# Performance work log

Hardware: AMD Instinct MI355X
Metric: run time of the kernel (lower is better)

The kernel has to match this reference:

```python
import jax, jax.numpy as jnp
import numpy as np

NEG_INF = -1e9


def setup_inputs() -> dict:
    key = jax.random.key(0)
    ks = jax.random.split(key, 12)
    B, Tq, Tki, E, D, M = 4, 2048, 2048, 1024, 128, 16384
    return {
        "x": jax.random.normal(ks[0], (B, Tq, E), jnp.float32),
        "ki": jax.random.normal(ks[1], (B, Tki, E), jnp.float32),
        "vi": jax.random.normal(ks[2], (B, Tki, E), jnp.float32),
        "mem_keys": jax.random.normal(ks[3], (B, M, D), jnp.float32),
        "mem_vals": jax.random.normal(ks[4], (B, M, D), jnp.float32),
        "Wq": jax.random.normal(ks[5], (E, D), jnp.float32) / np.sqrt(E),
        "bq": jax.random.normal(ks[6], (D,), jnp.float32) * 0.02,
        "Wk": jax.random.normal(ks[7], (E, D), jnp.float32) / np.sqrt(E),
        "bk": jax.random.normal(ks[8], (D,), jnp.float32) * 0.02,
        "Wv": jax.random.normal(ks[9], (E, D), jnp.float32) / np.sqrt(E),
        "bv": jax.random.normal(ks[10], (D,), jnp.float32) * 0.02,
        "gate": jax.random.normal(ks[11], (1,), jnp.float32),
        "idx": 3,
    }


def reference(x, ki, vi, mem_keys, mem_vals, Wq, bq, Wk, bk, Wv, bv, gate, idx):
    B, Tq, E = x.shape
    D = Wq.shape[1]
    top_k = 32
    q = x @ Wq + bq            # [B,Tq,D]
    k = x @ Wk + bk            # [B,Tq,D]
    v = x @ Wv + bv
    s = idx * D                # idx is a python int -> static slice
    k_full = jnp.concatenate([ki[:, :, s:s + D], k], axis=1)   # [B,Tk,D]
    v_full = jnp.concatenate([vi[:, :, s:s + D], v], axis=1)
    Tk = k_full.shape[1]
    # causal SDPA over prefix+current, offset diagonal Tk-Tq
    scores = jnp.einsum("bqd,bkd->bqk", q, k_full) / jnp.sqrt(jnp.float32(D))
    i = jnp.arange(Tq)[:, None]
    j = jnp.arange(Tk)[None, :]
    causal = j <= i + (Tk - Tq)
    scores = jnp.where(causal, scores, NEG_INF)
    att = jax.nn.softmax(scores, axis=-1)
    out = jnp.einsum("bqk,bkd->bqd", att, v_full)              # [B,Tq,D]
    # kNN memory attention: exact top-k inner-product search per query
    mem_scores = jnp.einsum("btd,bmd->btm", q, mem_keys)       # [B,Tq,M]
    _, top_idx = jax.lax.top_k(mem_scores, top_k)              # [B,Tq,K]
    gather = jax.vmap(lambda mem, ix: mem[ix])                 # per batch
    mem_k = gather(mem_keys, top_idx)                          # [B,Tq,K,D]
    mem_v = gather(mem_vals, top_idx)
    # note: original scales by sqrt(Cq)=sqrt(n_embd), not sqrt(head_size)
    mem_att = jax.nn.softmax(
        jnp.einsum("btd,btkd->btk", q, mem_k) / jnp.sqrt(jnp.float32(E)), axis=-1)
    mem_out = jnp.einsum("btk,btkd->btd", mem_att, mem_v)      # [B,Tq,D]
    md_out = out * gate + mem_out * (1.0 - gate)
    return md_out
```

## Files before the change

### kernel.cpp

```cpp
#include <hip/hip_runtime.h>


using bf16x8 = __attribute__((ext_vector_type(8))) short;
using f32x4  = __attribute__((ext_vector_type(4))) float;

typedef __attribute__((address_space(1))) const void GVoid;
typedef __attribute__((address_space(3))) void LVoid;
__device__ __forceinline__ void gl16(const ushort* g, ushort* l) {
  __builtin_amdgcn_global_load_lds((GVoid*)g, (LVoid*)l, 16, 0, 0);
}

__device__ __forceinline__ float bf2f(ushort h) {
  union { uint u; float f; } x; x.u = ((uint)h) << 16; return x.f;
}
__device__ __forceinline__ ushort f2bf(float f) {
  union { float f; uint u; } x; x.f = f;
  uint u = x.u;
  u += 0x7fffu + ((u >> 16) & 1u);
  return (ushort)(u >> 16);
}
__device__ __forceinline__ uint ord2(uint v) {
  uint lo = v & 0xffffu, hi = v >> 16;
  lo = (lo & 0x8000u) ? (0xffffu ^ lo) : (lo | 0x8000u);
  hi = (hi & 0x8000u) ? (0xffffu ^ hi) : (hi | 0x8000u);
  return lo | (hi << 16);
}

__global__ __launch_bounds__(256) void k_wt(const float* __restrict__ Wq,
                                            const float* __restrict__ Wk,
                                            const float* __restrict__ Wv,
                                            ushort* __restrict__ Wth,
                                            ushort* __restrict__ Wtlq) {
  int id = blockIdx.x * 256 + threadIdx.x;
  int z = id >> 17, r = id & 131071;
  int n = r >> 10, k = r & 1023;
  const float* W = (z == 1) ? Wk : (z == 2) ? Wv : Wq;
  float w = W[k * 128 + n];
  ushort h = f2bf(w);
  if (z < 3) Wth[id] = h;
  else       Wtlq[r] = f2bf(w - bf2f(h));
}

__global__ __launch_bounds__(256) void k_cvt8(const float* __restrict__ src,
                                              ushort* __restrict__ dst) {
  int id = blockIdx.x * 256 + threadIdx.x;
  size_t base = (size_t)id * 8;
  float4 a = *(const float4*)(src + base);
  float4 b = *(const float4*)(src + base + 4);
  bf16x8 r;
  r[0] = (short)f2bf(a.x); r[1] = (short)f2bf(a.y);
  r[2] = (short)f2bf(a.z); r[3] = (short)f2bf(a.w);
  r[4] = (short)f2bf(b.x); r[5] = (short)f2bf(b.y);
  r[6] = (short)f2bf(b.z); r[7] = (short)f2bf(b.w);
  *(bf16x8*)(dst + base) = r;
}

__global__ __launch_bounds__(256) void k_xsplit(const float* __restrict__ x,
                                                ushort* __restrict__ xh,
                                                ushort* __restrict__ xl) {
  int id = blockIdx.x * 256 + threadIdx.x;
  size_t base = (size_t)id * 8;
  float4 a = *(const float4*)(x + base);
  float4 b = *(const float4*)(x + base + 4);
  float xf[8] = {a.x, a.y, a.z, a.w, b.x, b.y, b.z, b.w};
  bf16x8 rh, rl;
#pragma unroll
  for (int j = 0; j < 8; ++j) {
    ushort h = f2bf(xf[j]);
    rh[j] = (short)h;
    rl[j] = (short)f2bf(xf[j] - bf2f(h));
  }
  *(bf16x8*)(xh + base) = rh;
  *(bf16x8*)(xl + base) = rl;
}

__global__ __launch_bounds__(256) void k_prefix(const float* __restrict__ ki,
                                                const float* __restrict__ vi,
                                                const int* __restrict__ idx,
                                                ushort* __restrict__ kfull,
                                                ushort* __restrict__ vfull) {
  int s = idx[0] * 128;
  int id = blockIdx.x * 256 + threadIdx.x;
  int d8 = (id & 15) * 8;
  int bt = id >> 4;
  int b = bt >> 11, t = bt & 2047;
  const float* kp = ki + (size_t)bt * 1024 + s + d8;
  const float* vp = vi + (size_t)bt * 1024 + s + d8;
  bf16x8 rk, rv;
#pragma unroll
  for (int j = 0; j < 8; ++j) { rk[j] = (short)f2bf(kp[j]); rv[j] = (short)f2bf(vp[j]); }
  size_t dst = ((size_t)b * 4096 + t) * 128 + d8;
  *(bf16x8*)(kfull + dst) = rk;
  *(bf16x8*)(vfull + dst) = rv;
}

__global__ __launch_bounds__(256) void k_qkv3(const ushort* __restrict__ xh,
                                              const ushort* __restrict__ xl,
                                              const ushort* __restrict__ Wth,
                                              const ushort* __restrict__ Wtlq,
                                              const float* __restrict__ bq,
                                              const float* __restrict__ bk,
                                              const float* __restrict__ bv,
                                              float* __restrict__ qex,
                                              ushort* __restrict__ kfull,
                                              ushort* __restrict__ vfull) {
  __shared__ ushort lds[2][16384];
  int z = blockIdx.z;
  int g = blockIdx.y;
  int m0 = blockIdx.x * 64;
  int tid = threadIdx.x;
  int w = tid >> 6, lane = tid & 63;
  int l15 = lane & 15, q8 = (lane >> 4) * 8;
  const ushort* Wz = Wth + (size_t)z * 131072;
  const ushort* xh_src = xh + (size_t)(m0 + w * 16 + l15) * 1024 + q8;
  const ushort* xl_src = xl + (size_t)(m0 + w * 16 + l15) * 1024 + q8;
  const ushort* wh_src = Wz   + (size_t)(g * 64 + w * 16 + l15) * 1024 + q8;
  const ushort* wl_src = Wtlq + (size_t)(g * 64 + w * 16 + l15) * 1024 + q8;
  int sb = w * 1024;

  f32x4 zero = {0.f, 0.f, 0.f, 0.f};
  f32x4 acc[4] = {zero, zero, zero, zero};

  {
    ushort* B = &lds[0][0];
    gl16(xh_src,      B + sb);
    gl16(xh_src + 32, B + sb + 512);
    gl16(wh_src,      B + 8192 + sb);
    gl16(wh_src + 32, B + 8192 + sb + 512);
    if (z == 0) {
      gl16(xl_src,      B + 4096 + sb);
      gl16(xl_src + 32, B + 4096 + sb + 512);
      gl16(wl_src,      B + 12288 + sb);
      gl16(wl_src + 32, B + 12288 + sb + 512);
    }
  }
  __syncthreads();
  int bf = 0;
  for (int t16 = 0; t16 < 16; ++t16) {
    if (t16 < 15) {
      int k0 = t16 * 64 + 64;
      ushort* B = &lds[bf ^ 1][0];
      gl16(xh_src + k0,      B + sb);
      gl16(xh_src + k0 + 32, B + sb + 512);
      gl16(wh_src + k0,      B + 8192 + sb);
      gl16(wh_src + k0 + 32, B + 8192 + sb + 512);
      if (z == 0) {
        gl16(xl_src + k0,      B + 4096 + sb);
        gl16(xl_src + k0 + 32, B + 4096 + sb + 512);
        gl16(wl_src + k0,      B + 12288 + sb);
        gl16(wl_src + k0 + 32, B + 12288 + sb + 512);
      }
    }
    const ushort* B = &lds[bf][0];
    int lo = lane * 8;
    if (z == 0) {
#pragma unroll
      for (int kc = 0; kc < 2; ++kc) {
        bf16x8 ah = *(const bf16x8*)(B + (w * 2 + kc) * 512 + lo);
        bf16x8 al = *(const bf16x8*)(B + 4096 + (w * 2 + kc) * 512 + lo);
#pragma unroll
        for (int cc = 0; cc < 4; ++cc) {
          bf16x8 bh = *(const bf16x8*)(B + 8192 + (cc * 2 + kc) * 512 + lo);
          bf16x8 bl = *(const bf16x8*)(B + 12288 + (cc * 2 + kc) * 512 + lo);
          acc[cc] = __builtin_amdgcn_mfma_f32_16x16x32_bf16(ah, bh, acc[cc], 0, 0, 0);
          acc[cc] = __builtin_amdgcn_mfma_f32_16x16x32_bf16(ah, bl, acc[cc], 0, 0, 0);
          acc[cc] = __builtin_amdgcn_mfma_f32_16x16x32_bf16(al, bh, acc[cc], 0, 0, 0);
        }
      }
    } else {
#pragma unroll
      for (int kc = 0; kc < 2; ++kc) {
        bf16x8 ah = *(const bf16x8*)(B + (w * 2 + kc) * 512 + lo);
#pragma unroll
        for (int cc = 0; cc < 4; ++cc) {
          bf16x8 bh = *(const bf16x8*)(B + 8192 + (cc * 2 + kc) * 512 + lo);
          acc[cc] = __builtin_amdgcn_mfma_f32_16x16x32_bf16(ah, bh, acc[cc], 0, 0, 0);
        }
      }
    }
    __syncthreads();
    bf ^= 1;
  }

  const float* bias = (z == 0) ? bq : (z == 1) ? bk : bv;
  int mrow = m0 + w * 16 + (lane >> 4) * 4;
#pragma unroll
  for (int cc = 0; cc < 4; ++cc) {
    int n = g * 64 + cc * 16 + l15;
    float bb = bias[n];
#pragma unroll
    for (int r = 0; r < 4; ++r) {
      int m = mrow + r;
      float val = acc[cc][r] + bb;
      if (z == 0) {
        qex[(size_t)m * 128 + n] = val;
      } else {
        int b2 = m >> 11, tt = m & 2047;
        size_t o = ((size_t)b2 * 4096 + 2048 + tt) * 128 + n;
        if (z == 1) kfull[o] = f2bf(val); else vfull[o] = f2bf(val);
      }
    }
  }
}

__global__ __launch_bounds__(256) void k_vt(const ushort* __restrict__ vfull,
                                            ushort* __restrict__ Vt) {
  __shared__ ushort lds[64][136];
  int blk = blockIdx.x;
  int b = blk >> 6, t0 = (blk & 63) * 64;
  int t = threadIdx.x;
#pragma unroll
  for (int p = 0; p < 4; ++p) {
    int ch = p * 256 + t;
    int row = ch >> 4, c8 = (ch & 15) * 8;
    uint4 v = *(const uint4*)(vfull + ((size_t)b * 4096 + t0 + row) * 128 + c8);
    *(uint4*)(&lds[row][c8]) = v;
  }
  __syncthreads();
#pragma unroll
  for (int p = 0; p < 8; ++p) {
    int q = p * 256 + t;
    int d = q >> 4, t4 = (q & 15) * 4;
    ushort4 o;
    o.x = lds[t4 + 0][d]; o.y = lds[t4 + 1][d];
    o.z = lds[t4 + 2][d]; o.w = lds[t4 + 3][d];
    *(ushort4*)(Vt + ((size_t)b * 128 + d) * 4096 + t0 + t4) = o;
  }
}

__global__ __launch_bounds__(256) void k_scores(const float* __restrict__ A,
                                                const ushort* __restrict__ Bm,
                                                ushort* __restrict__ S,
                                                int N, int nslice, int causalOff,
                                                long sA, long sB, long sS) {
  __shared__ ushort Bt[64 * 136];
  int q0 = blockIdx.x * 64;
  int ns0 = blockIdx.y * nslice;
  int nend = ns0 + nslice; if (nend > N) nend = N;
  int climit = q0 + 64 + causalOff; if (nend > climit) nend = climit;
  if (ns0 >= nend) return;
  int zb = blockIdx.z;
  const float*  Ab = A  + (size_t)zb * sA;
  const ushort* Bb = Bm + (size_t)zb * sB;
  ushort* Sb = S + (size_t)zb * sS;
  int t = threadIdx.x, lane = t & 63, wv = t >> 6;
  int l15 = lane & 15, q8 = (lane >> 4) * 8;
  const float* Arow = Ab + (size_t)(q0 + wv * 16 + l15) * 128 + q8;
  bf16x8 af[4];
#pragma unroll
  for (int kc = 0; kc < 4; ++kc)
#pragma unroll
    for (int j = 0; j < 8; ++j) af[kc][j] = (short)f2bf(Arow[kc * 32 + j]);
  for (int n0 = ns0; n0 < nend; n0 += 64) {
#pragma unroll
    for (int p = 0; p < 4; ++p) {
      int ch = p * 256 + t;
      int row = ch >> 4, c8 = (ch & 15) * 8;
      uint4 v = *(const uint4*)(Bb + (size_t)(n0 + row) * 128 + c8);
      *(uint4*)(&Bt[row * 136 + c8]) = v;
    }
    __syncthreads();
    f32x4 zero = {0.f, 0.f, 0.f, 0.f};
    f32x4 acc[4] = {zero, zero, zero, zero};
#pragma unroll
    for (int h = 0; h < 4; ++h) {
#pragma unroll
      for (int kc = 0; kc < 4; ++kc) {
        bf16x8 bfr = *(const bf16x8*)(&Bt[(h * 16 + l15) * 136 + kc * 32 + q8]);
        acc[h] = __builtin_amdgcn_mfma_f32_16x16x32_bf16(af[kc], bfr, acc[h], 0, 0, 0);
      }
    }
    int qq = q0 + wv * 16 + (lane >> 4) * 4;
#pragma unroll
    for (int h = 0; h < 4; ++h)
#pragma unroll
      for (int r = 0; r < 4; ++r)
        Sb[(size_t)(qq + r) * N + (n0 + h * 16 + l15)] = f2bf(acc[h][r]);
    __syncthreads();
  }
}

__global__ __launch_bounds__(256) void k_softmax(ushort* __restrict__ S) {
  int rid = blockIdx.x;
  int i = rid & 2047;
  ushort* row = S + (size_t)rid * 4096;
  int w = i + 2049;
  int t = threadIdx.x;
  const float scale = 0.08838834764831845f;
  float v[16];
  float mx = -1e30f;
#pragma unroll
  for (int c = 0; c < 16; ++c) {
    int e = c * 256 + t;
    float f = -1e30f;
    if (e < w) f = bf2f(row[e]) * scale;
    v[c] = f;
    mx = fmaxf(mx, f);
  }
  __shared__ float red[4];
#pragma unroll
  for (int off = 32; off; off >>= 1) mx = fmaxf(mx, __shfl_xor(mx, off));
  if ((t & 63) == 0) red[t >> 6] = mx;
  __syncthreads();
  mx = fmaxf(fmaxf(red[0], red[1]), fmaxf(red[2], red[3]));
  __syncthreads();
  float ex[16];
  float sum = 0.f;
#pragma unroll
  for (int c = 0; c < 16; ++c) {
    int e = c * 256 + t;
    ex[c] = (e < w) ? __expf(v[c] - mx) : 0.f;
    sum += ex[c];
  }
#pragma unroll
  for (int off = 32; off; off >>= 1) sum += __shfl_xor(sum, off);
  if ((t & 63) == 0) red[t >> 6] = sum;
  __syncthreads();
  sum = red[0] + red[1] + red[2] + red[3];
  float inv = 1.f / sum;
#pragma unroll
  for (int c = 0; c < 16; ++c) {
    int e = c * 256 + t;
    row[e] = f2bf(ex[c] * inv);
  }
}

__global__ __launch_bounds__(128) void k_pv(const ushort* __restrict__ P,
                                            const ushort* __restrict__ Vt,
                                            float* __restrict__ O) {
  __shared__ ushort lds[2][6144];
  int b = blockIdx.z;
  int d0 = blockIdx.y * 64;
  int q0 = blockIdx.x * 32;
  int t = threadIdx.x, lane = t & 63, w = t >> 6;
  int l15 = lane & 15, q8 = (lane >> 4) * 8;
  const ushort* Pq = P + ((size_t)b * 2048 + q0) * 4096;
  const ushort* Vb = Vt + (size_t)b * 128 * 4096;
  const ushort* p_src  = Pq + (size_t)(w * 16 + l15) * 4096 + q8;
  const ushort* v_src0 = Vb + (size_t)(d0 + (w * 2 + 0) * 16 + l15) * 4096 + q8;
  const ushort* v_src1 = Vb + (size_t)(d0 + (w * 2 + 1) * 16 + l15) * 4096 + q8;
  int kend = q0 + 32 + 2048; if (kend > 4096) kend = 4096;
  int ksteps = (kend + 63) >> 6;

  f32x4 zero = {0.f, 0.f, 0.f, 0.f};
  f32x4 acc[4] = {zero, zero, zero, zero};

  {
    ushort* B = &lds[0][0];
    gl16(p_src,       B + (w * 2 + 0) * 512);
    gl16(p_src + 32,  B + (w * 2 + 1) * 512);
    gl16(v_src0,      B + 2048 + ((w * 2 + 0) * 2 + 0) * 512);
    gl16(v_src0 + 32, B + 2048 + ((w * 2 + 0) * 2 + 1) * 512);
    gl16(v_src1,      B + 2048 + ((w * 2 + 1) * 2 + 0) * 512);
    gl16(v_src1 + 32, B + 2048 + ((w * 2 + 1) * 2 + 1) * 512);
  }
  __syncthreads();
  int bf = 0;
  for (int st = 0; st < ksteps; ++st) {
    if (st + 1 < ksteps) {
      int k0 = st * 64 + 64;
      ushort* B = &lds[bf ^ 1][0];
      gl16(p_src + k0,       B + (w * 2 + 0) * 512);
      gl16(p_src + k0 + 32,  B + (w * 2 + 1) * 512);
      gl16(v_src0 + k0,      B + 2048 + ((w * 2 + 0) * 2 + 0) * 512);
      gl16(v_src0 + k0 + 32, B + 2048 + ((w * 2 + 0) * 2 + 1) * 512);
      gl16(v_src1 + k0,      B + 2048 + ((w * 2 + 1) * 2 + 0) * 512);
      gl16(v_src1 + k0 + 32, B + 2048 + ((w * 2 + 1) * 2 + 1) * 512);
    }
    const ushort* B = &lds[bf][0];
    int lo = lane * 8;
#pragma unroll
    for (int kc = 0; kc < 2; ++kc) {
      bf16x8 af = *(const bf16x8*)(B + (w * 2 + kc) * 512 + lo);
#pragma unroll
      for (int nc = 0; nc < 4; ++nc) {
        bf16x8 bfr = *(const bf16x8*)(B + 2048 + (nc * 2 + kc) * 512 + lo);
        acc[nc] = __builtin_amdgcn_mfma_f32_16x16x32_bf16(af, bfr, acc[nc], 0, 0, 0);
      }
    }
    __syncthreads();
    bf ^= 1;
  }

  size_t ob = ((size_t)b * 2048 + q0 + w * 16 + (lane >> 4) * 4) * 128;
#pragma unroll
  for (int nc = 0; nc < 4; ++nc)
#pragma unroll
    for (int r = 0; r < 4; ++r)
      O[ob + (size_t)r * 128 + d0 + nc * 16 + l15] = acc[nc][r];
}

__global__ __launch_bounds__(256) void k_topk(const ushort* __restrict__ Sall,
                                              const float* __restrict__ qf32b,
                                              const float* __restrict__ memk,
                                              const float* __restrict__ memv,
                                              float* __restrict__ mout) {
  __shared__ uint sred[32];
  __shared__ float qf[128];
  __shared__ uint cidx[384];
  __shared__ float csc[384];
  __shared__ unsigned long long ckey[384];
  __shared__ uint selIdx[32];
  __shared__ float selS[32];
  __shared__ float obuf[256];
  __shared__ int nC;

  int i = blockIdx.x;
  const ushort* Srow = Sall + (size_t)i * 16384;
  int t = threadIdx.x;
  int wv = t >> 6, lane = t & 63;
  if (t < 128) qf[t] = qf32b[(size_t)i * 128 + t];
  if (t == 0) nC = 0;

  uint keys[32];
#pragma unroll
  for (int c = 0; c < 8; ++c) {
    int base = (c * 256 + t) * 8;
    uint4 rv = *(const uint4*)(Srow + base);
    keys[c * 4 + 0] = ord2(rv.x);
    keys[c * 4 + 1] = ord2(rv.y);
    keys[c * 4 + 2] = ord2(rv.z);
    keys[c * 4 + 3] = ord2(rv.w);
  }
  uint mymax = 0;
#pragma unroll
  for (int r = 0; r < 32; ++r) {
    uint v = keys[r];
    uint hi = v >> 16, lo = v & 0xffffu;
    uint mm = hi > lo ? hi : lo;
    mymax = mm > mymax ? mm : mymax;
  }
#pragma unroll
  for (int off = 32; off; off >>= 1) {
    uint o = __shfl_xor(mymax, off);
    mymax = o > mymax ? o : mymax;
  }
  if (lane == 0) sred[wv] = mymax;
  __syncthreads();
  uint M = sred[0];
  { uint a = sred[1]; M = a > M ? a : M;
    a = sred[2]; M = a > M ? a : M;
    a = sred[3]; M = a > M ? a : M; }
  __syncthreads();

  uint T;
  uint MbCur = M >> 5;
  uint carry = 0;
  while (true) {
    uint h0 = 0, h1 = 0;
#pragma unroll
    for (int r = 0; r < 32; ++r) {
      uint v = keys[r];
      uint blo = MbCur - ((v & 0xffffu) >> 5);
      uint bhi = MbCur - (v >> 21);
      if (blo < 8u) { uint a = 1u << ((blo & 3u) << 3); if (blo < 4u) h0 += a; else h1 += a; }
      if (bhi < 8u) { uint a = 1u << ((bhi & 3u) << 3); if (bhi < 4u) h0 += a; else h1 += a; }
    }
    uint c8[8] = {h0 & 255u, (h0 >> 8) & 255u, (h0 >> 16) & 255u, h0 >> 24,
                  h1 & 255u, (h1 >> 8) & 255u, (h1 >> 16) & 255u, h1 >> 24};
#pragma unroll
    for (int b = 0; b < 8; ++b)
#pragma unroll
      for (int off = 32; off; off >>= 1) c8[b] += __shfl_xor(c8[b], off);
    if (lane == 0) {
#pragma unroll
      for (int b = 0; b < 8; ++b) sred[wv * 8 + b] = c8[b];
    }
    __syncthreads();
    uint cum = carry; int bstar = -1;
#pragma unroll
    for (int b = 0; b < 8; ++b) {
      uint tb = sred[b] + sred[8 + b] + sred[16 + b] + sred[24 + b];
      cum += tb;
      if (bstar < 0 && cum >= 64u) bstar = b;
    }
    if (bstar >= 0) { T = (MbCur - (uint)bstar) << 5; break; }
    carry = cum;
    MbCur -= 8u;
    __syncthreads();
  }

#pragma unroll
  for (int r = 0; r < 32; ++r) {
    uint v = keys[r];
    int base = ((r >> 2) * 256 + t) * 8 + ((r & 3) * 2);
    if ((v & 0xffffu) >= T) { int p = atomicAdd(&nC, 1); if (p < 384) cidx[p] = (uint)base; }
    if ((v >> 16) >= T)     { int p = atomicAdd(&nC, 1); if (p < 384) cidx[p] = (uint)(base + 1); }
  }
  __syncthreads();
  int C = nC; if (C > 384) C = 384;
  {
    float qa = qf[lane * 2], qb = qf[lane * 2 + 1];
    for (int j0 = wv; j0 < C; j0 += 32) {
      float2 pp[8];
      float s[8];
#pragma unroll
      for (int u = 0; u < 8; ++u) {
        int j = j0 + u * 4;
        if (j < C) pp[u] = *(const float2*)(memk + (size_t)cidx[j] * 128 + lane * 2);
      }
#pragma unroll
      for (int u = 0; u < 8; ++u) {
        int j = j0 + u * 4;
        s[u] = (j < C) ? (qa * pp[u].x + qb * pp[u].y) : 0.f;
      }
#pragma unroll
      for (int off = 32; off; off >>= 1) {
#pragma unroll
        for (int u = 0; u < 8; ++u) s[u] += __shfl_xor(s[u], off);
      }
      if (lane == 0) {
#pragma unroll
        for (int u = 0; u < 8; ++u) {
          int j = j0 + u * 4;
          if (j < C) csc[j] = s[u];
        }
      }
    }
  }
  __syncthreads();
  for (int j = t; j < C; j += 256) {
    uint sb2 = __float_as_uint(csc[j]);
    uint o = (sb2 & 0x80000000u) ? ~sb2 : (sb2 | 0x80000000u);
    ckey[j] = ((unsigned long long)o << 32) | (uint)(~cidx[j]);
  }
  __syncthreads();
  for (int j = t; j < C; j += 256) {
    unsigned long long my = ckey[j];
    int rank = 0;
    for (int l = 0; l < C; ++l) rank += (ckey[l] > my) ? 1 : 0;
    if (rank < 32) { selS[rank] = csc[j]; selIdx[rank] = cidx[j]; }
  }
  __syncthreads();
  if (wv == 0) {
    float sc = (lane < 32) ? selS[lane] * 0.03125f : -1e30f;
    float mx = sc;
#pragma unroll
    for (int off = 32; off; off >>= 1) mx = fmaxf(mx, __shfl_xor(mx, off));
    float ex = (lane < 32) ? __expf(sc - mx) : 0.f;
    float Z = ex;
#pragma unroll
    for (int off = 32; off; off >>= 1) Z += __shfl_xor(Z, off);
    if (lane < 32) selS[lane] = ex / Z;
  }
  __syncthreads();
  {
    int d = t & 127, half = t >> 7;
    float vv[16];
#pragma unroll
    for (int u = 0; u < 16; ++u)
      vv[u] = memv[(size_t)selIdx[half * 16 + u] * 128 + d];
    float acc = 0.f;
#pragma unroll
    for (int u = 0; u < 16; ++u)
      acc += selS[half * 16 + u] * vv[u];
    obuf[t] = acc;
  }
  __syncthreads();
  if (t < 128) mout[(size_t)i * 128 + t] = obuf[t] + obuf[t + 128];
}

__global__ __launch_bounds__(256) void k_mix(const float* __restrict__ a,
                                             const float* __restrict__ b,
                                             const float* __restrict__ gate,
                                             float* __restrict__ out) {
  int id = blockIdx.x * 256 + threadIdx.x;
  float g = gate[0];
  float4 va = ((const float4*)a)[id];
  float4 vb = ((const float4*)b)[id];
  float4 o;
  o.x = va.x * g + vb.x * (1.f - g);
  o.y = va.y * g + vb.y * (1.f - g);
  o.z = va.z * g + vb.z * (1.f - g);
  o.w = va.w * g + vb.w * (1.f - g);
  ((float4*)out)[id] = o;
}

extern "C" void kernel_launch(void* const* d_in, const int* in_sizes, int n_in,
                              void* d_out, int out_size, void* d_ws, size_t ws_size,
                              hipStream_t stream) {
  const float* x    = (const float*)d_in[0];
  const float* ki   = (const float*)d_in[1];
  const float* vi   = (const float*)d_in[2];
  const float* mk   = (const float*)d_in[3];
  const float* mv   = (const float*)d_in[4];
  const float* Wq   = (const float*)d_in[5];
  const float* bq   = (const float*)d_in[6];
  const float* Wk   = (const float*)d_in[7];
  const float* bk   = (const float*)d_in[8];
  const float* Wv   = (const float*)d_in[9];
  const float* bv   = (const float*)d_in[10];
  const float* gate = (const float*)d_in[11];
  const int*   idx  = (const int*)d_in[12];

  char* ws = (char*)d_ws;
  ushort* Sbuf  = (ushort*)(ws);
  ushort* xh    = (ushort*)(ws);
  ushort* xl    = (ushort*)(ws + 16777216);
  float*  qex   = (float*) (ws + 67108864);
  ushort* kfull = (ushort*)(ws + 71303168);
  ushort* vfull = (ushort*)(ws + 75497472);
  ushort* Vt    = (ushort*)(ws + 79691776);
  ushort* mkb   = (ushort*)(ws + 83886080);
  ushort* Wth   = (ushort*)(ws + 100663296);
  ushort* Wtlq  = (ushort*)(ws + 101449728);
  float*  osdpa = (float*) (ws + 101711872);
  float*  mout  = (float*) (ws + 105906176);

  k_wt<<<2048, 256, 0, stream>>>(Wq, Wk, Wv, Wth, Wtlq);
  k_cvt8<<<4096, 256, 0, stream>>>(mk, mkb);
  k_xsplit<<<4096, 256, 0, stream>>>(x, xh, xl);
  k_prefix<<<512, 256, 0, stream>>>(ki, vi, idx, kfull, vfull);

  k_qkv3<<<dim3(128, 2, 3), 256, 0, stream>>>(xh, xl, Wth, Wtlq, bq, bk, bv,
                                              qex, kfull, vfull);
  k_vt<<<256, 256, 0, stream>>>(vfull, Vt);

  k_scores<<<dim3(32, 4, 4), 256, 0, stream>>>(qex, kfull, Sbuf,
                                               4096, 1024, 2048,
                                               (long)2048 * 128, (long)4096 * 128,
                                               (long)2048 * 4096);
  k_softmax<<<8192, 256, 0, stream>>>(Sbuf);
  k_pv<<<dim3(64, 2, 4), 128, 0, stream>>>(Sbuf, Vt, osdpa);

  for (int b = 0; b < 4; ++b) {
    k_scores<<<dim3(32, 8, 1), 256, 0, stream>>>(qex + (size_t)b * 2048 * 128,
                                                 mkb + (size_t)b * 16384 * 128,
                                                 Sbuf, 16384, 2048, (1 << 28),
                                                 0, 0, 0);
    k_topk<<<2048, 256, 0, stream>>>(Sbuf, qex + (size_t)b * 2048 * 128,
                                     mk + (size_t)b * 16384 * 128,
                                     mv + (size_t)b * 16384 * 128,
                                     mout + (size_t)b * 2048 * 128);
  }

  k_mix<<<1024, 256, 0, stream>>>(osdpa, mout, gate, (float*)d_out);
}
```

Measured before the change: 710.3 us.

## Split top-k kernel into candidate selection and attention kernels with ballot compaction

Splits the fused top-k kernel into a threshold/candidate selection kernel and a separate rescoring/attention kernel, with candidates passed through a global buffer. Each half should use fewer registers and less LDS, which may raise occupancy. Also replaces per-element LDS atomics with wave ballot plus prefix popcount compaction, rewrites ord2 as branchless bit ops, and unrolls the rank-counting loop by 8. The cost is an extra launch per batch and a global round trip for the candidate lists.

```diff
diff --git a/kernel.cpp b/kernel.cpp
--- a/kernel.cpp
+++ b/kernel.cpp
@@ -20,10 +20,9 @@
   return (ushort)(u >> 16);
 }
 __device__ __forceinline__ uint ord2(uint v) {
-  uint lo = v & 0xffffu, hi = v >> 16;
-  lo = (lo & 0x8000u) ? (0xffffu ^ lo) : (lo | 0x8000u);
-  hi = (hi & 0x8000u) ? (0xffffu ^ hi) : (hi | 0x8000u);
-  return lo | (hi << 16);
+  uint s = (v >> 15) & 0x00010001u;
+  uint t = (s << 15) - s;
+  return v ^ t ^ 0x80008000u;
 }
 
 __global__ __launch_bounds__(256) void k_wt(const float* __restrict__ Wq,
@@ -390,12 +389,122 @@
       O[ob + (size_t)r * 128 + d0 + nc * 16 + l15] = acc[nc][r];
 }
 
-__global__ __launch_bounds__(256) void k_topk(const ushort* __restrict__ Sall,
-                                              const float* __restrict__ qf32b,
-                                              const float* __restrict__ memk,
-                                              const float* __restrict__ memv,
-                                              float* __restrict__ mout) {
+__global__ __launch_bounds__(256) void k_topksel(const ushort* __restrict__ Sall,
+                                                 uint* __restrict__ cand,
+                                                 int* __restrict__ ccnt) {
   __shared__ uint sred[32];
+  __shared__ int nC;
+  int i = blockIdx.x;
+  const ushort* Srow = Sall + (size_t)i * 16384;
+  int t = threadIdx.x;
+  int wv = t >> 6, lane = t & 63;
+  if (t == 0) nC = 0;
+
+  uint4 rv[8];
+#pragma unroll
+  for (int c = 0; c < 8; ++c)
+    rv[c] = *(const uint4*)(Srow + (c * 256 + t) * 8);
+  uint keys[32];
+#pragma unroll
+  for (int c = 0; c < 8; ++c) {
+    keys[c * 4 + 0] = ord2(rv[c].x);
+    keys[c * 4 + 1] = ord2(rv[c].y);
+    keys[c * 4 + 2] = ord2(rv[c].z);
+    keys[c * 4 + 3] = ord2(rv[c].w);
+  }
+  uint mymax = 0;
+#pragma unroll
+  for (int r = 0; r < 32; ++r) {
+    uint v = keys[r];
+    uint hi = v >> 16, lo = v & 0xffffu;
+    uint mm = hi > lo ? hi : lo;
+    mymax = mm > mymax ? mm : mymax;
+  }
+#pragma unroll
+  for (int off = 32; off; off >>= 1) {
+    uint o = __shfl_xor(mymax, off);
+    mymax = o > mymax ? o : mymax;
+  }
+  if (lane == 0) sred[wv] = mymax;
+  __syncthreads();
+  uint M = sred[0];
+  { uint a = sred[1]; M = a > M ? a : M;
+    a = sred[2]; M = a > M ? a : M;
+    a = sred[3]; M = a > M ? a : M; }
+  __syncthreads();
+
+  uint T;
+  uint MbCur = M >> 5;
+  uint carry = 0;
+  while (true) {
+    uint h0 = 0, h1 = 0;
+#pragma unroll
+    for (int r = 0; r < 32; ++r) {
+      uint v = keys[r];
+      uint blo = MbCur - ((v & 0xffffu) >> 5);
+      uint bhi = MbCur - (v >> 21);
+      if (blo < 8u) { uint a = 1u << ((blo & 3u) << 3); if (blo < 4u) h0 += a; else h1 += a; }
+      if (bhi < 8u) { uint a = 1u << ((bhi & 3u) << 3); if (bhi < 4u) h0 += a; else h1 += a; }
+    }
+    uint c8[8] = {h0 & 255u, (h0 >> 8) & 255u, (h0 >> 16) & 255u, h0 >> 24,
+                  h1 & 255u, (h1 >> 8) & 255u, (h1 >> 16) & 255u, h1 >> 24};
+#pragma unroll
+    for (int b = 0; b < 8; ++b)
+#pragma unroll
+      for (int off = 32; off; off >>= 1) c8[b] += __shfl_xor(c8[b], off);
+    if (lane == 0) {
+#pragma unroll
+      for (int b = 0; b < 8; ++b) sred[wv * 8 + b] = c8[b];
+    }
+    __syncthreads();
+    uint cum = carry; int bstar = -1;
+#pragma unroll
+    for (int b = 0; b < 8; ++b) {
+      uint tb = sred[b] + sred[8 + b] + sred[16 + b] + sred[24 + b];
+      cum += tb;
+      if (bstar < 0 && cum >= 64u) bstar = b;
+    }
+    if (bstar >= 0) { T = (MbCur - (uint)bstar) << 5; break; }
+    carry = cum;
+    MbCur -= 8u;
+    __syncthreads();
+  }
+
+  uint* crow = cand + (size_t)i * 384;
+  ulong below = (lane == 0) ? 0ull : ((~0ull) >> (64 - lane));
+#pragma unroll
+  for (int r = 0; r < 32; ++r) {
+    uint v = keys[r];
+    bool clo = (v & 0xffffu) >= T;
+    bool chi = (v >> 16) >= T;
+    unsigned long long mlo = __ballot(clo);
+    unsigned long long mhi = __ballot(chi);
+    int cnt = __popcll(mlo) + __popcll(mhi);
+    if (cnt) {
+      int old = 0;
+      if (lane == 0) old = atomicAdd(&nC, cnt);
+      int base = __shfl(old, 0);
+      int bidx = ((r >> 2) * 256 + t) * 8 + ((r & 3) * 2);
+      if (clo) {
+        int p = base + __popcll(mlo & below);
+        if (p < 384) crow[p] = (uint)bidx;
+      }
+      if (chi) {
+        int p = base + __popcll(mlo) + __popcll(mhi & below);
+        if (p < 384) crow[p] = (uint)(bidx + 1);
+      }
+    }
+  }
+  __syncthreads();
+  if (t == 0) { int C = nC; ccnt[i] = C > 384 ? 384 : C; }
+}
+
+__global__ __launch_bounds__(256) void k_topkatt(const uint* __restrict__ cand,
+                                                 const int* __restrict__ ccnt,
+                                                 const float* __restrict__ qf32b,
+                                                 const float* __restrict__ memk,
+                                                 const float* __restrict__ memv,
+                                                 float* __restrict__ mout) {
   __shared__ float qf[128];
   __shared__ uint cidx[384];
   __shared__ float csc[384];
@@ -403,92 +512,19 @@
   __shared__ uint selIdx[32];
   __shared__ float selS[32];
   __shared__ float obuf[256];
-  __shared__ int nC;
 
   int i = blockIdx.x;
-  const ushort* Srow = Sall + (size_t)i * 16384;
   int t = threadIdx.x;
   int wv = t >> 6, lane = t & 63;
   if (t < 128) qf[t] = qf32b[(size_t)i * 128 + t];
-  if (t == 0) nC = 0;
-
-  uint keys[32];
-#pragma unroll
-  for (int c = 0; c < 8; ++c) {
-    int base = (c * 256 + t) * 8;
-    uint4 rv = *(const uint4*)(Srow + base);
-    keys[c * 4 + 0] = ord2(rv.x);
-    keys[c * 4 + 1] = ord2(rv.y);
-    keys[c * 4 + 2] = ord2(rv.z);
-    keys[c * 4 + 3] = ord2(rv.w);
-  }
-  uint mymax = 0;
-#pragma unroll
-  for (int r = 0; r < 32; ++r) {
-    uint v = keys[r];
-    uint hi = v >> 16, lo = v & 0xffffu;
-    uint mm = hi > lo ? hi : lo;
-    mymax = mm > mymax ? mm : mymax;
-  }
-#pragma unroll
-  for (int off = 32; off; off >>= 1) {
-    uint o = __shfl_xor(mymax, off);
-    mymax = o > mymax ? o : mymax;
-  }
-  if (lane == 0) sred[wv] = mymax;
-  __syncthreads();
-  uint M = sred[0];
-  { uint a = sred[1]; M = a > M ? a : M;
-    a = sred[2]; M = a > M ? a : M;
-    a = sred[3]; M = a > M ? a : M; }
-  __syncthreads();
-
-  uint T;
-  uint MbCur = M >> 5;
-  uint carry = 0;
-  while (true) {
-    uint h0 = 0, h1 = 0;
-#pragma unroll
-    for (int r = 0; r < 32; ++r) {
-      uint v = keys[r];
-      uint blo = MbCur - ((v & 0xffffu) >> 5);
-      uint bhi = MbCur - (v >> 21);
-      if (blo < 8u) { uint a = 1u << ((blo & 3u) << 3); if (blo < 4u) h0 += a; else h1 += a; }
-      if (bhi < 8u) { uint a = 1u << ((bhi & 3u) << 3); if (bhi < 4u) h0 += a; else h1 += a; }
-    }
-    uint c8[8] = {h0 & 255u, (h0 >> 8) & 255u, (h0 >> 16) & 255u, h0 >> 24,
-                  h1 & 255u, (h1 >> 8) & 255u, (h1 >> 16) & 255u, h1 >> 24};
-#pragma unroll
-    for (int b = 0; b < 8; ++b)
-#pragma unroll
-      for (int off = 32; off; off >>= 1) c8[b] += __shfl_xor(c8[b], off);
-    if (lane == 0) {
-#pragma unroll
-      for (int b = 0; b < 8; ++b) sred[wv * 8 + b] = c8[b];
-    }
-    __syncthreads();
-    uint cum = carry; int bstar = -1;
-#pragma unroll
-    for (int b = 0; b < 8; ++b) {
-      uint tb = sred[b] + sred[8 + b] + sred[16 + b] + sred[24 + b];
-      cum += tb;
-      if (bstar < 0 && cum >= 64u) bstar = b;
-    }
-    if (bstar >= 0) { T = (MbCur - (uint)bstar) << 5; break; }
-    carry = cum;
-    MbCur -= 8u;
-    __syncthreads();
-  }
-
-#pragma unroll
-  for (int r = 0; r < 32; ++r) {
-    uint v = keys[r];
-    int base = ((r >> 2) * 256 + t) * 8 + ((r & 3) * 2);
-    if ((v & 0xffffu) >= T) { int p = atomicAdd(&nC, 1); if (p < 384) cidx[p] = (uint)base; }
-    if ((v >> 16) >= T)     { int p = atomicAdd(&nC, 1); if (p < 384) cidx[p] = (uint)(base + 1); }
-  }
-  __syncthreads();
-  int C = nC; if (C > 384) C = 384;
+  int C = ccnt[i];
+  const uint* crow = cand + (size_t)i * 384;
+  for (int j = t; j < 384; j += 256) {
+    cidx[j] = (j < C) ? crow[j] : 0u;
+    ckey[j] = 0ull;
+  }
+  __syncthreads();
+
   {
     float qa = qf[lane * 2], qb = qf[lane * 2 + 1];
     for (int j0 = wv; j0 < C; j0 += 32) {
@@ -525,10 +561,18 @@
     ckey[j] = ((unsigned long long)o << 32) | (uint)(~cidx[j]);
   }
   __syncthreads();
+  int Cpad = (C + 7) & ~7;
   for (int j = t; j < C; j += 256) {
     unsigned long long my = ckey[j];
     int rank = 0;
-    for (int l = 0; l < C; ++l) rank += (ckey[l] > my) ? 1 : 0;
+    for (int l = 0; l < Cpad; l += 8) {
+      unsigned long long k0 = ckey[l + 0], k1 = ckey[l + 1];
+      unsigned long long k2 = ckey[l + 2], k3 = ckey[l + 3];
+      unsigned long long k4 = ckey[l + 4], k5 = ckey[l + 5];
+      unsigned long long k6 = ckey[l + 6], k7 = ckey[l + 7];
+      rank += (k0 > my) + (k1 > my) + (k2 > my) + (k3 > my);
+      rank += (k4 > my) + (k5 > my) + (k6 > my) + (k7 > my);
+    }
     if (rank < 32) { selS[rank] = csc[j]; selIdx[rank] = cidx[j]; }
   }
   __syncthreads();
@@ -606,6 +650,8 @@
   ushort* Wtlq  = (ushort*)(ws + 101449728);
   float*  osdpa = (float*) (ws + 101711872);
   float*  mout  = (float*) (ws + 105906176);
+  uint*   cand  = (uint*)  (ws + 110100480);
+  int*    ccnt  = (int*)   (ws + 113246208);
 
   k_wt<<<2048, 256, 0, stream>>>(Wq, Wk, Wv, Wth, Wtlq);
   k_cvt8<<<4096, 256, 0, stream>>>(mk, mkb);
@@ -628,10 +674,12 @@
                                                  mkb + (size_t)b * 16384 * 128,
                                                  Sbuf, 16384, 2048, (1 << 28),
                                                  0, 0, 0);
-    k_topk<<<2048, 256, 0, stream>>>(Sbuf, qex + (size_t)b * 2048 * 128,
-                                     mk + (size_t)b * 16384 * 128,
-                                     mv + (size_t)b * 16384 * 128,
-                                     mout + (size_t)b * 2048 * 128);
+    k_topksel<<<2048, 256, 0, stream>>>(Sbuf, cand, ccnt);
+    k_topkatt<<<2048, 256, 0, stream>>>(cand, ccnt,
+                                        qex + (size_t)b * 2048 * 128,
+                                        mk + (size_t)b * 16384 * 128,
+                                        mv + (size_t)b * 16384 * 128,
+                                        mout + (size_t)b * 2048 * 128);
   }
 
   k_mix<<<1024, 256, 0, stream>>>(osdpa, mout, gate, (float*)d_out);
```

Result: slower. 744.0 us (+4.7%).
